# Kernel optimization log

Hardware: AMD Instinct MI355X
Metric: run time of the kernel (lower is better)

The kernel has to match this reference:

```python
import jax, jax.numpy as jnp
import numpy as np

N_NODES = 50000
N_EDGES = 800000
IN_CH = 128
HID = 32
HEADS = 4
OUT_CH = 8
NEG_SLOPE = 0.2  # PyG GATConv default


def gat_conv(x, edge_index_sl, W, a_src, a_dst, b, heads, out_ch):
    """One PyG-style GATConv (self-loops already appended to edge_index_sl).
    x: [N, F_in], W: [F_in, heads*out_ch], a_src/a_dst: [heads, out_ch], b: [heads*out_ch].
    """
    N = x.shape[0]
    src, dst = edge_index_sl[0], edge_index_sl[1]
    h = (x @ W).reshape(N, heads, out_ch)                 # [N, H, C]
    alpha_src = jnp.sum(h * a_src, axis=-1)               # [N, H]
    alpha_dst = jnp.sum(h * a_dst, axis=-1)               # [N, H]
    logits = jax.nn.leaky_relu(alpha_src[src] + alpha_dst[dst], NEG_SLOPE)  # [E, H]
    # segment softmax over edges grouped by destination node
    seg_max = jax.ops.segment_max(logits, dst, num_segments=N)  # [N, H]
    e = jnp.exp(logits - seg_max[dst])
    seg_sum = jax.ops.segment_sum(e, dst, num_segments=N)       # [N, H]
    alpha = e / seg_sum[dst]                                    # [E, H]
    msg = h[src] * alpha[:, :, None]                            # [E, H, C]
    out = jax.ops.segment_sum(msg, dst, num_segments=N)         # [N, H, C]
    return out.reshape(N, heads * out_ch) + b


def setup_inputs() -> dict:
    key = jax.random.key(0)
    ks = jax.random.split(key, 10)
    glorot = lambda k, shape: jax.random.normal(k, shape, jnp.float32) * jnp.sqrt(2.0 / (shape[0] + shape[-1]))
    x = jax.random.normal(ks[0], (N_NODES, IN_CH), jnp.float32)
    edge_index = jax.random.randint(ks[1], (2, N_EDGES), 0, N_NODES, dtype=jnp.int64)
    return {
        "x": x,
        "edge_index": edge_index,
        "W1": glorot(ks[2], (IN_CH, HEADS * HID)),
        "a_src1": glorot(ks[3], (HEADS, HID)),
        "a_dst1": glorot(ks[4], (HEADS, HID)),
        "b1": jnp.zeros((HEADS * HID,), jnp.float32),
        "W2": glorot(ks[5], (HEADS * HID, OUT_CH)),
        "a_src2": glorot(ks[6], (1, OUT_CH)),
        "a_dst2": glorot(ks[7], (1, OUT_CH)),
        "b2": jnp.zeros((OUT_CH,), jnp.float32),
    }


def reference(x, edge_index, W1, a_src1, a_dst1, b1, W2, a_src2, a_dst2, b2):
    N = x.shape[0]
    loops = jnp.arange(N, dtype=edge_index.dtype)
    ei = jnp.concatenate([edge_index, jnp.stack([loops, loops])], axis=1)  # add self-loops
    # dropout is inference no-op
    h = gat_conv(x, ei, W1, a_src1, a_dst1, b1, HEADS, HID)
    h = jax.nn.elu(h)
    out = gat_conv(h, ei, W2, a_src2, a_dst2, b2, 1, OUT_CH)
    return out  # [N, OUT_CH]
```

## Files before the change

### kernel.cpp

```cpp
#include <hip/hip_runtime.h>
#include <hip/hip_bf16.h>
#include <math.h>

#define NN 50000
#define NE 800000
#define ET 850000
#define FIN 128
#define HTOT 128
#define OUTC 8
#define NB ((NN + 255) / 256)
#define XLD 132

__device__ __forceinline__ float lrelu(float v){ return v > 0.f ? v : 0.2f*v; }
__device__ __forceinline__ float eluf(float v){ return v > 0.f ? v : expm1f(v); }

__device__ __forceinline__ unsigned pack_bf16(float a, float b){
  __hip_bfloat16 ha = __float2bfloat16(a);
  __hip_bfloat16 hb = __float2bfloat16(b);
  const unsigned short ua = *(const unsigned short*)&ha;
  const unsigned short ub = *(const unsigned short*)&hb;
  return ((unsigned)ub << 16) | (unsigned)ua;
}
__device__ __forceinline__ float bf_lo(unsigned u){ return __int_as_float((int)(u << 16)); }
__device__ __forceinline__ float bf_hi(unsigned u){ return __int_as_float((int)(u & 0xffff0000u)); }

__global__ __launch_bounds__(256) void k_gemm(
    const float* __restrict__ x, const float* __restrict__ W1,
    const float* __restrict__ a_src1, const float* __restrict__ a_dst1,
    unsigned* __restrict__ h1b, float* __restrict__ as1, float* __restrict__ ad1)
{
  __shared__ float xl[64 * XLD];
  const int t = threadIdx.x;
  const int r0 = blockIdx.x * 64;

  #pragma unroll
  for (int i = 0; i < 8; ++i) {
    const int f   = i*256 + t;
    const int row = f >> 5;
    const int c4  = f & 31;
    const int gr  = r0 + row;
    float4 v = make_float4(0.f,0.f,0.f,0.f);
    if (gr < NN) v = *(const float4*)&x[(size_t)gr*FIN + c4*4];
    *(float4*)&xl[row*XLD + c4*4] = v;
  }
  __syncthreads();

  const int tx = t & 15, ty = t >> 4;
  const int c0a = tx*4;
  const int c0b = 64 + tx*4;

  float acc[4][8];
  #pragma unroll
  for (int i=0;i<4;++i)
    #pragma unroll
    for (int j=0;j<8;++j) acc[i][j] = 0.f;

  for (int k = 0; k < 128; k += 4) {
    float4 xv[4];
    #pragma unroll
    for (int i=0;i<4;++i)
      xv[i] = *(const float4*)&xl[(ty*4+i)*XLD + k];
    #pragma unroll
    for (int kk = 0; kk < 4; ++kk) {
      const float4 wa = *(const float4*)&W1[(size_t)(k+kk)*128 + c0a];
      const float4 wb = *(const float4*)&W1[(size_t)(k+kk)*128 + c0b];
      #pragma unroll
      for (int i=0;i<4;++i) {
        const float xk = (kk==0)?xv[i].x:(kk==1)?xv[i].y:(kk==2)?xv[i].z:xv[i].w;
        acc[i][0] += xk*wa.x; acc[i][1] += xk*wa.y; acc[i][2] += xk*wa.z; acc[i][3] += xk*wa.w;
        acc[i][4] += xk*wb.x; acc[i][5] += xk*wb.y; acc[i][6] += xk*wb.z; acc[i][7] += xk*wb.w;
      }
    }
  }

  #pragma unroll
  for (int i=0;i<4;++i) {
    const int gr = r0 + ty*4 + i;
    if (gr < NN) {
      uint2 ua, ub;
      ua.x = pack_bf16(acc[i][0], acc[i][1]);
      ua.y = pack_bf16(acc[i][2], acc[i][3]);
      ub.x = pack_bf16(acc[i][4], acc[i][5]);
      ub.y = pack_bf16(acc[i][6], acc[i][7]);
      *(uint2*)&h1b[(size_t)gr*64 + tx*2]      = ua;
      *(uint2*)&h1b[(size_t)gr*64 + 32 + tx*2] = ub;
    }
  }

  float sa[4], sb[4], da[4], db[4];
  {
    const float4 v0 = *(const float4*)&a_src1[c0a];
    const float4 v1 = *(const float4*)&a_src1[c0b];
    const float4 v2 = *(const float4*)&a_dst1[c0a];
    const float4 v3 = *(const float4*)&a_dst1[c0b];
    sa[0]=v0.x; sa[1]=v0.y; sa[2]=v0.z; sa[3]=v0.w;
    sb[0]=v1.x; sb[1]=v1.y; sb[2]=v1.z; sb[3]=v1.w;
    da[0]=v2.x; da[1]=v2.y; da[2]=v2.z; da[3]=v2.w;
    db[0]=v3.x; db[1]=v3.y; db[2]=v3.z; db[3]=v3.w;
  }
  const int ha = tx >> 3;
  #pragma unroll
  for (int i=0;i<4;++i) {
    float psa = 0.f, pda = 0.f, psb = 0.f, pdb = 0.f;
    #pragma unroll
    for (int j=0;j<4;++j) {
      psa += acc[i][j]  *sa[j]; pda += acc[i][j]  *da[j];
      psb += acc[i][4+j]*sb[j]; pdb += acc[i][4+j]*db[j];
    }
    psa += __shfl_xor(psa,1); psa += __shfl_xor(psa,2); psa += __shfl_xor(psa,4);
    pda += __shfl_xor(pda,1); pda += __shfl_xor(pda,2); pda += __shfl_xor(pda,4);
    psb += __shfl_xor(psb,1); psb += __shfl_xor(psb,2); psb += __shfl_xor(psb,4);
    pdb += __shfl_xor(pdb,1); pdb += __shfl_xor(pdb,2); pdb += __shfl_xor(pdb,4);
    const int gr = r0 + ty*4 + i;
    if ((tx & 7) == 0 && gr < NN) {
      as1[(size_t)gr*4 + ha]     = psa;
      ad1[(size_t)gr*4 + ha]     = pda;
      as1[(size_t)gr*4 + ha + 2] = psb;
      ad1[(size_t)gr*4 + ha + 2] = pdb;
    }
  }
}

__global__ __launch_bounds__(256) void k_hist(const int* __restrict__ ei,
                                              unsigned* __restrict__ counts)
{
  const int e = blockIdx.x*256 + threadIdx.x;
  if (e >= ET) return;
  const int d = (e < NE) ? ei[NE + e] : (e - NE);
  atomicAdd(&counts[d], 1u);
}

__global__ __launch_bounds__(256) void k_scan_part(const unsigned* __restrict__ counts,
                                                   unsigned* __restrict__ bsum)
{
  const int idx = blockIdx.x*256 + threadIdx.x;
  unsigned v = (idx < NN) ? counts[idx] : 0u;
  #pragma unroll
  for (int o = 1; o < 64; o <<= 1) v += __shfl_xor(v, o);
  __shared__ unsigned wsum[4];
  const int lane = threadIdx.x & 63, wid = threadIdx.x >> 6;
  if (lane == 0) wsum[wid] = v;
  __syncthreads();
  if (threadIdx.x == 0) bsum[blockIdx.x] = wsum[0]+wsum[1]+wsum[2]+wsum[3];
}

__global__ __launch_bounds__(256) void k_scan_mid(const unsigned* __restrict__ bsum,
                                                  unsigned* __restrict__ boff)
{
  const int t = threadIdx.x;
  const unsigned v = (t < NB) ? bsum[t] : 0u;
  unsigned inc = v;
  const int lane = t & 63, wid = t >> 6;
  #pragma unroll
  for (int o = 1; o < 64; o <<= 1) {
    const unsigned u = __shfl_up(inc, o, 64);
    if (lane >= o) inc += u;
  }
  __shared__ unsigned wsum[4], woff[4];
  if (lane == 63) wsum[wid] = inc;
  __syncthreads();
  if (t == 0) { unsigned run = 0; for (int i=0;i<4;++i){ woff[i]=run; run+=wsum[i]; } }
  __syncthreads();
  if (t < NB) boff[t] = woff[wid] + inc - v;
}

__global__ __launch_bounds__(256) void k_scan_exp(const unsigned* __restrict__ counts,
    const unsigned* __restrict__ boff,
    unsigned* __restrict__ rowptr, unsigned* __restrict__ fill)
{
  const int idx = blockIdx.x*256 + threadIdx.x;
  const unsigned v = (idx < NN) ? counts[idx] : 0u;
  unsigned inc = v;
  const int lane = threadIdx.x & 63, wid = threadIdx.x >> 6;
  #pragma unroll
  for (int o = 1; o < 64; o <<= 1) {
    const unsigned u = __shfl_up(inc, o, 64);
    if (lane >= o) inc += u;
  }
  __shared__ unsigned wsum[4], woff[4];
  if (lane == 63) wsum[wid] = inc;
  __syncthreads();
  if (threadIdx.x == 0) { unsigned run = 0; for (int i=0;i<4;++i){ woff[i]=run; run+=wsum[i]; } }
  __syncthreads();
  const unsigned exc = boff[blockIdx.x] + woff[wid] + inc - v;
  if (idx < NN) { rowptr[idx] = exc; fill[idx] = exc; }
  if (idx == 0) rowptr[NN] = ET;
}

__global__ __launch_bounds__(256) void k_scatter(const int* __restrict__ ei,
    unsigned* __restrict__ fill, unsigned* __restrict__ srcs)
{
  const int e = blockIdx.x*256 + threadIdx.x;
  if (e >= ET) return;
  int s, d;
  if (e < NE) { s = ei[e]; d = ei[NE + e]; } else { s = e - NE; d = s; }
  const unsigned pos = atomicAdd(&fill[d], 1u);
  srcs[pos] = (unsigned)s;
}

__global__ __launch_bounds__(256) void k_agg1(
    const unsigned* __restrict__ rowptr, const unsigned* __restrict__ srcs,
    const unsigned* __restrict__ h1b, const float* __restrict__ as1,
    const float* __restrict__ ad1, const float* __restrict__ b1,
    const float* __restrict__ W2, const float* __restrict__ a_src2,
    const float* __restrict__ a_dst2,
    float* __restrict__ g, float* __restrict__ as2v, float* __restrict__ ad2v)
{
  __shared__ unsigned sh_src[4][64];
  __shared__ float    sh_w[4][64][4];
  const int lane = threadIdx.x & 63;
  const int wv   = threadIdx.x >> 6;
  const int n = blockIdx.x*4 + wv;
  if (n >= NN) return;
  const unsigned beg = rowptr[n], end = rowptr[n+1];
  const float4 ad = *(const float4*)&ad1[(size_t)n*4];
  const int h = lane >> 4;

  float acc0 = 0.f, acc1 = 0.f;
  float sw0 = 0.f, sw1 = 0.f, sw2 = 0.f, sw3 = 0.f;

  for (unsigned base = beg; base < end; base += 64) {
    const unsigned i = base + (unsigned)lane;
    if (i < end) {
      const unsigned s = srcs[i];
      const float4 as = *(const float4*)&as1[(size_t)s*4];
      const float w0 = __expf(lrelu(as.x + ad.x));
      const float w1 = __expf(lrelu(as.y + ad.y));
      const float w2 = __expf(lrelu(as.z + ad.z));
      const float w3 = __expf(lrelu(as.w + ad.w));
      sw0 += w0; sw1 += w1; sw2 += w2; sw3 += w3;
      sh_src[wv][lane] = s;
      *(float4*)&sh_w[wv][lane][0] = make_float4(w0,w1,w2,w3);
    }
    __builtin_amdgcn_wave_barrier();

    const int cnt = (int)((end - base < 64u) ? (end - base) : 64u);
    int j = 0;
    for (; j + 7 < cnt; j += 8) {
      unsigned sv[8]; float wvv[8]; unsigned uv[8];
      #pragma unroll
      for (int q=0;q<8;++q) { sv[q] = sh_src[wv][j+q]; wvv[q] = sh_w[wv][j+q][h]; }
      #pragma unroll
      for (int q=0;q<8;++q) uv[q] = h1b[(size_t)sv[q]*64 + lane];
      #pragma unroll
      for (int q=0;q<8;++q) {
        acc0 += wvv[q]*bf_lo(uv[q]);
        acc1 += wvv[q]*bf_hi(uv[q]);
      }
    }
    for (; j < cnt; ++j) {
      const unsigned s0 = sh_src[wv][j];
      const float w0 = sh_w[wv][j][h];
      const unsigned u = h1b[(size_t)s0*64 + lane];
      acc0 += w0*bf_lo(u); acc1 += w0*bf_hi(u);
    }
    __builtin_amdgcn_wave_barrier();
  }

  #pragma unroll
  for (int o = 1; o < 64; o <<= 1) {
    sw0 += __shfl_xor(sw0, o); sw1 += __shfl_xor(sw1, o);
    sw2 += __shfl_xor(sw2, o); sw3 += __shfl_xor(sw3, o);
  }
  const float swh = (h==0)?sw0:(h==1)?sw1:(h==2)?sw2:sw3;
  const float inv = 1.0f / swh;

  const int c0 = lane*2;
  const float2 bb = *(const float2*)&b1[c0];
  const float e0 = eluf(acc0*inv + bb.x);
  const float e1 = eluf(acc1*inv + bb.y);

  const float4 wa0 = *(const float4*)&W2[(size_t)c0*8];
  const float4 wa1 = *(const float4*)&W2[(size_t)c0*8 + 4];
  const float4 wb0 = *(const float4*)&W2[(size_t)(c0+1)*8];
  const float4 wb1 = *(const float4*)&W2[(size_t)(c0+1)*8 + 4];
  float p0 = e0*wa0.x + e1*wb0.x;
  float p1 = e0*wa0.y + e1*wb0.y;
  float p2 = e0*wa0.z + e1*wb0.z;
  float p3 = e0*wa0.w + e1*wb0.w;
  float p4 = e0*wa1.x + e1*wb1.x;
  float p5 = e0*wa1.y + e1*wb1.y;
  float p6 = e0*wa1.z + e1*wb1.z;
  float p7 = e0*wa1.w + e1*wb1.w;
  #pragma unroll
  for (int o = 1; o < 64; o <<= 1) {
    p0 += __shfl_xor(p0, o); p1 += __shfl_xor(p1, o);
    p2 += __shfl_xor(p2, o); p3 += __shfl_xor(p3, o);
    p4 += __shfl_xor(p4, o); p5 += __shfl_xor(p5, o);
    p6 += __shfl_xor(p6, o); p7 += __shfl_xor(p7, o);
  }
  if (lane == 0) {
    *(float4*)&g[(size_t)n*8]     = make_float4(p0,p1,p2,p3);
    *(float4*)&g[(size_t)n*8 + 4] = make_float4(p4,p5,p6,p7);
    const float s2 = p0*a_src2[0]+p1*a_src2[1]+p2*a_src2[2]+p3*a_src2[3]
                   + p4*a_src2[4]+p5*a_src2[5]+p6*a_src2[6]+p7*a_src2[7];
    const float d2 = p0*a_dst2[0]+p1*a_dst2[1]+p2*a_dst2[2]+p3*a_dst2[3]
                   + p4*a_dst2[4]+p5*a_dst2[5]+p6*a_dst2[6]+p7*a_dst2[7];
    as2v[n] = s2; ad2v[n] = d2;
  }
}

__global__ __launch_bounds__(256) void k_agg2(
    const unsigned* __restrict__ rowptr, const unsigned* __restrict__ srcs,
    const float* __restrict__ g, const float* __restrict__ as2v,
    const float* __restrict__ ad2v, const float* __restrict__ b2,
    float* __restrict__ out)
{
  const int lane = threadIdx.x & 63;
  const int n = blockIdx.x*4 + (threadIdx.x >> 6);
  if (n >= NN) return;
  const unsigned beg = rowptr[n], end = rowptr[n+1];
  const float adv = ad2v[n];

  float a0=0.f,a1=0.f,a2=0.f,a3=0.f,a4=0.f,a5=0.f,a6=0.f,a7=0.f,sw=0.f;
  for (unsigned i = beg + lane; i < end; i += 64) {
    const unsigned s = srcs[i];
    const float w = __expf(lrelu(as2v[s] + adv));
    sw += w;
    const float4 ga = *(const float4*)&g[(size_t)s*8];
    const float4 gb = *(const float4*)&g[(size_t)s*8 + 4];
    a0 += w*ga.x; a1 += w*ga.y; a2 += w*ga.z; a3 += w*ga.w;
    a4 += w*gb.x; a5 += w*gb.y; a6 += w*gb.z; a7 += w*gb.w;
  }
  #pragma unroll
  for (int o = 1; o < 64; o <<= 1) {
    sw += __shfl_xor(sw, o);
    a0 += __shfl_xor(a0, o); a1 += __shfl_xor(a1, o);
    a2 += __shfl_xor(a2, o); a3 += __shfl_xor(a3, o);
    a4 += __shfl_xor(a4, o); a5 += __shfl_xor(a5, o);
    a6 += __shfl_xor(a6, o); a7 += __shfl_xor(a7, o);
  }
  if (lane == 0) {
    const float inv = 1.0f / sw;
    *(float4*)&out[(size_t)n*8] =
        make_float4(a0*inv + b2[0], a1*inv + b2[1], a2*inv + b2[2], a3*inv + b2[3]);
    *(float4*)&out[(size_t)n*8 + 4] =
        make_float4(a4*inv + b2[4], a5*inv + b2[5], a6*inv + b2[6], a7*inv + b2[7]);
  }
}

extern "C" void kernel_launch(void* const* d_in, const int* in_sizes, int n_in,
                              void* d_out, int out_size, void* d_ws, size_t ws_size,
                              hipStream_t stream) {
  const float* x      = (const float*)d_in[0];
  const int*   ei     = (const int*)d_in[1];
  const float* W1     = (const float*)d_in[2];
  const float* a_src1 = (const float*)d_in[3];
  const float* a_dst1 = (const float*)d_in[4];
  const float* b1     = (const float*)d_in[5];
  const float* W2     = (const float*)d_in[6];
  const float* a_src2 = (const float*)d_in[7];
  const float* a_dst2 = (const float*)d_in[8];
  const float* b2     = (const float*)d_in[9];
  float* out = (float*)d_out;

  char* ws = (char*)d_ws;
  unsigned* h1b    = (unsigned*)(ws + 0);
  float*    as1    = (float*)(ws + 25600000);
  float*    ad1    = (float*)(ws + 26400000);
  float*    g      = (float*)(ws + 27200000);
  float*    as2v   = (float*)(ws + 28800000);
  float*    ad2v   = (float*)(ws + 29000000);
  unsigned* counts = (unsigned*)(ws + 29200000);
  unsigned* rowptr = (unsigned*)(ws + 29400000);
  unsigned* fill   = (unsigned*)(ws + 29600016);
  unsigned* srcs   = (unsigned*)(ws + 29800016);
  unsigned* bsum   = (unsigned*)(ws + 33200016);
  unsigned* boff   = (unsigned*)(ws + 33201600);

  hipMemsetAsync(counts, 0, NN*sizeof(unsigned), stream);

  k_gemm<<<(NN + 63)/64, 256, 0, stream>>>(x, W1, a_src1, a_dst1, h1b, as1, ad1);
  k_hist<<<(ET + 255)/256, 256, 0, stream>>>(ei, counts);
  k_scan_part<<<NB, 256, 0, stream>>>(counts, bsum);
  k_scan_mid<<<1, 256, 0, stream>>>(bsum, boff);
  k_scan_exp<<<NB, 256, 0, stream>>>(counts, boff, rowptr, fill);
  k_scatter<<<(ET + 255)/256, 256, 0, stream>>>(ei, fill, srcs);
  k_agg1<<<(NN + 3)/4, 256, 0, stream>>>(rowptr, srcs, h1b, as1, ad1, b1,
                                         W2, a_src2, a_dst2, g, as2v, ad2v);
  k_agg2<<<(NN + 3)/4, 256, 0, stream>>>(rowptr, srcs, g, as2v, ad2v, b2, out);
}
```

Before: 301.6 us.

## Split each node's edge range across two waves in first aggregation

```diff
diff --git a/kernel.cpp b/kernel.cpp
--- a/kernel.cpp
+++ b/kernel.cpp
@@ -208,11 +208,17 @@
 {
   __shared__ unsigned sh_src[4][64];
   __shared__ float    sh_w[4][64][4];
+  __shared__ float    sh_acc[2][128];
+  __shared__ float    sh_sw[2][4];
   const int lane = threadIdx.x & 63;
   const int wv   = threadIdx.x >> 6;
-  const int n = blockIdx.x*4 + wv;
-  if (n >= NN) return;
-  const unsigned beg = rowptr[n], end = rowptr[n+1];
+  const int slot = wv >> 1;
+  const int half = wv & 1;
+  const int n = blockIdx.x*2 + slot;
+  const unsigned nbeg = rowptr[n], nend = rowptr[n+1];
+  const unsigned mid = nbeg + ((nend - nbeg) >> 1);
+  const unsigned beg = half ? mid : nbeg;
+  const unsigned end = half ? nend : mid;
   const float4 ad = *(const float4*)&ad1[(size_t)n*4];
   const int h = lane >> 4;
 
@@ -237,11 +243,14 @@
     const int cnt = (int)((end - base < 64u) ? (end - base) : 64u);
     int j = 0;
     for (; j + 7 < cnt; j += 8) {
-      unsigned sv[8]; float wvv[8]; unsigned uv[8];
+      unsigned off[8]; float wvv[8]; unsigned uv[8];
       #pragma unroll
-      for (int q=0;q<8;++q) { sv[q] = sh_src[wv][j+q]; wvv[q] = sh_w[wv][j+q][h]; }
+      for (int q=0;q<8;++q) {
+        off[q] = (sh_src[wv][j+q] << 6) | (unsigned)lane;
+        wvv[q] = sh_w[wv][j+q][h];
+      }
       #pragma unroll
-      for (int q=0;q<8;++q) uv[q] = h1b[(size_t)sv[q]*64 + lane];
+      for (int q=0;q<8;++q) uv[q] = h1b[off[q]];
       #pragma unroll
       for (int q=0;q<8;++q) {
         acc0 += wvv[q]*bf_lo(uv[q]);
@@ -249,9 +258,9 @@
       }
     }
     for (; j < cnt; ++j) {
-      const unsigned s0 = sh_src[wv][j];
+      const unsigned off = (sh_src[wv][j] << 6) | (unsigned)lane;
       const float w0 = sh_w[wv][j][h];
-      const unsigned u = h1b[(size_t)s0*64 + lane];
+      const unsigned u = h1b[off];
       acc0 += w0*bf_lo(u); acc1 += w0*bf_hi(u);
     }
     __builtin_amdgcn_wave_barrier();
@@ -262,6 +271,23 @@
     sw0 += __shfl_xor(sw0, o); sw1 += __shfl_xor(sw1, o);
     sw2 += __shfl_xor(sw2, o); sw3 += __shfl_xor(sw3, o);
   }
+
+  if (half) {
+    sh_acc[slot][lane*2]     = acc0;
+    sh_acc[slot][lane*2 + 1] = acc1;
+    if (lane == 0) {
+      sh_sw[slot][0] = sw0; sh_sw[slot][1] = sw1;
+      sh_sw[slot][2] = sw2; sh_sw[slot][3] = sw3;
+    }
+  }
+  __syncthreads();
+  if (half) return;
+
+  acc0 += sh_acc[slot][lane*2];
+  acc1 += sh_acc[slot][lane*2 + 1];
+  sw0 += sh_sw[slot][0]; sw1 += sh_sw[slot][1];
+  sw2 += sh_sw[slot][2]; sw3 += sh_sw[slot][3];
+
   const float swh = (h==0)?sw0:(h==1)?sw1:(h==2)?sw2:sw3;
   const float inv = 1.0f / swh;
 
@@ -376,7 +402,7 @@
   k_scan_mid<<<1, 256, 0, stream>>>(bsum, boff);
   k_scan_exp<<<NB, 256, 0, stream>>>(counts, boff, rowptr, fill);
   k_scatter<<<(ET + 255)/256, 256, 0, stream>>>(ei, fill, srcs);
-  k_agg1<<<(NN + 3)/4, 256, 0, stream>>>(rowptr, srcs, h1b, as1, ad1, b1,
-                                         W2, a_src2, a_dst2, g, as2v, ad2v);
+  k_agg1<<<NN/2, 256, 0, stream>>>(rowptr, srcs, h1b, as1, ad1, b1,
+                                   W2, a_src2, a_dst2, g, as2v, ad2v);
   k_agg2<<<(NN + 3)/4, 256, 0, stream>>>(rowptr, srcs, g, as2v, ad2v, b2, out);
 }
```

Result: slower. 321.6 us (+6.6%).
